# Kernel tuning notes

Measured on AMD Instinct MI355X. Metric: run time of the kernel, lower is better.

Reference implementation:

```python
import jax, jax.numpy as jnp
import numpy as np

NUM_QUERIES = 300

def setup_inputs() -> dict:
    key = jax.random.key(0)
    k1, k2, k3, k4 = jax.random.split(key, 4)
    B, A, L, H = 32, 8400, 80, 256
    return {
        "enc_outputs_class": jax.random.normal(k1, (B, A, L), dtype=jnp.float32),
        "enc_outputs_coord_logits_plus_anchors": jax.random.normal(k2, (B, A, 4), dtype=jnp.float32),
        "output_memory": jax.random.normal(k3, (B, A, H), dtype=jnp.float32),
        "sources_last_element": jax.random.normal(k4, (B, H, 20, 20), dtype=jnp.float32),
    }

def reference(enc_outputs_class, enc_outputs_coord_logits_plus_anchors, output_memory, sources_last_element):
    # enc_outputs_class: [B, A, L]; reduce class dim, top-k over anchors A.
    cls_max = jnp.max(enc_outputs_class, axis=-1)                      # [B, A]
    _, topk_ind = jax.lax.top_k(cls_max, NUM_QUERIES)                  # [B, Q], sorted desc
    idx = topk_ind[:, :, None]                                         # [B, Q, 1]

    def gather(data):  # per-batch gather along anchor axis
        return jnp.take_along_axis(data, idx, axis=1)

    reference_points_unact = gather(enc_outputs_coord_logits_plus_anchors)  # [B, Q, 4]
    enc_topk_logits = gather(enc_outputs_class)                             # [B, Q, L]
    enc_topk_bboxes = jax.nn.sigmoid(reference_points_unact)               # [B, Q, 4]

    # learn_initial_query=False: target comes from gathered encoder memory (stop-grad)
    target = jax.lax.stop_gradient(gather(output_memory))                   # [B, Q, H]
    init_reference_points = jax.lax.stop_gradient(reference_points_unact)  # [B, Q, 4]
    return (init_reference_points, target, enc_topk_logits, enc_topk_bboxes)
```

## Files before the change

### kernel.cpp

```cpp
#include <hip/hip_runtime.h>
#include <stdint.h>

#define BATCH 32
#define NA    8400
#define NL    80
#define NH    256
#define NK    300
#define NBIN  8192

#define OUT0 0
#define OUT1 38400
#define OUT2 2496000
#define OUT3 3264000

__device__ __forceinline__ unsigned mapf(float f) {
    unsigned u = __float_as_uint(f);
    return (u & 0x80000000u) ? ~u : (u | 0x80000000u);
}

__global__ __launch_bounds__(256) void cls_max_kernel(const float* __restrict__ cls,
                                                      unsigned* __restrict__ out_u) {
    int tid = threadIdx.x;
    int row = blockIdx.x * 64 + (tid >> 2);
    int sub = tid & 3;
    if (row >= BATCH * NA) return;
    const float4* p = (const float4*)(cls + (size_t)row * NL);
    float m = -3.4e38f;
#pragma unroll
    for (int q = 0; q < 5; ++q) {
        float4 v = p[sub + q * 4];
        m = fmaxf(m, fmaxf(fmaxf(v.x, v.y), fmaxf(v.z, v.w)));
    }
    m = fmaxf(m, __shfl_xor(m, 1));
    m = fmaxf(m, __shfl_xor(m, 2));
    if (sub == 0) out_u[row] = mapf(m);
}

__global__ __launch_bounds__(1024) void select_gather_kernel(
        const unsigned* __restrict__ u_in,
        const float*    __restrict__ cls,
        const float*    __restrict__ coord,
        const float*    __restrict__ mem,
        float*          __restrict__ out) {
    __shared__ unsigned hist[NBIN];
    __shared__ unsigned long long keys[1024];
    __shared__ int ord[NK];
    __shared__ unsigned wsum[16], wsuf[16];
    __shared__ unsigned s_thr, s_count;

    int tid  = threadIdx.x;
    int lane = tid & 63;
    int wid  = tid >> 6;
    int b    = blockIdx.x >> 3;
    int sub  = blockIdx.x & 7;
    const unsigned* ub = u_in + b * NA;

    for (int i = tid; i < NBIN; i += 1024) hist[i] = 0;
    if (tid == 0) s_count = 0;
    __syncthreads();

    unsigned v[9];
#pragma unroll
    for (int k = 0; k < 9; ++k) {
        int i = tid + k * 1024;
        v[k] = (i < NA) ? ub[i] : 0u;
    }
#pragma unroll
    for (int k = 0; k < 9; ++k) {
        int i = tid + k * 1024;
        if (i < NA) atomicAdd(&hist[v[k] >> 19], 1u);
    }
    __syncthreads();

    unsigned base = tid * 8;
    unsigned h[8];
#pragma unroll
    for (int j = 0; j < 8; ++j) h[j] = hist[base + j];
    unsigned L = 0;
#pragma unroll
    for (int j = 0; j < 8; ++j) L += h[j];
    unsigned s = L;
#pragma unroll
    for (int off = 1; off < 64; off <<= 1) {
        unsigned t = __shfl_down(s, off);
        if (lane + off < 64) s += t;
    }
    if (lane == 0) wsum[wid] = s;
    __syncthreads();
    if (tid == 0) {
        unsigned acc = 0;
        for (int w = 15; w >= 0; --w) { acc += wsum[w]; wsuf[w] = acc; }
    }
    __syncthreads();
    unsigned above = (wid < 15 ? wsuf[wid + 1] : 0u) + (s - L);
    unsigned acc = above;
#pragma unroll
    for (int j = 7; j >= 0; --j) {
        unsigned S = acc + h[j];
        if (S >= (unsigned)NK && acc < (unsigned)NK) s_thr = base + (unsigned)j;
        acc = S;
    }
    __syncthreads();

    unsigned T = s_thr;
#pragma unroll
    for (int k = 0; k < 9; ++k) {
        int i = tid + k * 1024;
        if (i < NA && (v[k] >> 19) >= T) {
            unsigned pos = atomicAdd(&s_count, 1u);
            if (pos < 1024) keys[pos] = ((unsigned long long)(~v[k]) << 32) | (unsigned)i;
        }
    }
    __syncthreads();

    unsigned count = s_count < 1024u ? s_count : 1024u;
    if (tid < (int)count) {
        unsigned long long mykey = keys[tid];
        int rank = 0;
        for (unsigned j = 0; j < count; ++j) rank += (keys[j] < mykey);
        if (rank < NK) ord[rank] = (int)(mykey & 0xFFFFFFFFull);
    }
    __syncthreads();

    for (int q = sub + 8 * wid; q < NK; q += 8 * 16) {
        int idx = ord[q];
        size_t srow = (size_t)b * NA + (size_t)idx;
        size_t drow = (size_t)b * NK + (size_t)q;

        const float4* msrc = (const float4*)(mem + srow * NH);
        float4*       mdst = (float4*)(out + OUT1 + drow * NH);
        mdst[lane] = msrc[lane];

        if (lane < 20) {
            const float4* lsrc = (const float4*)(cls + srow * NL);
            float4*       ldst = (float4*)(out + OUT2 + drow * NL);
            ldst[lane] = lsrc[lane];
        }
        if (lane == 0) {
            float4 c = ((const float4*)(coord + srow * 4))[0];
            ((float4*)(out + OUT0 + drow * 4))[0] = c;
            float4 sg;
            sg.x = 1.0f / (1.0f + __expf(-c.x));
            sg.y = 1.0f / (1.0f + __expf(-c.y));
            sg.z = 1.0f / (1.0f + __expf(-c.z));
            sg.w = 1.0f / (1.0f + __expf(-c.w));
            ((float4*)(out + OUT3 + drow * 4))[0] = sg;
        }
    }
}

extern "C" void kernel_launch(void* const* d_in, const int* in_sizes, int n_in,
                              void* d_out, int out_size, void* d_ws, size_t ws_size,
                              hipStream_t stream) {
    const float* cls   = (const float*)d_in[0];
    const float* coord = (const float*)d_in[1];
    const float* mem   = (const float*)d_in[2];

    unsigned* ws_u = (unsigned*)d_ws;
    float*    out  = (float*)d_out;

    cls_max_kernel<<<(BATCH * NA) / 64, 256, 0, stream>>>(cls, ws_u);
    select_gather_kernel<<<BATCH * 8, 1024, 0, stream>>>(ws_u, cls, coord, mem, out);
}
```

Before: 34.73 us.

## Fuse class-max and select-gather into one cooperative kernel with grid sync

Merges the per-anchor class-max kernel into the selection/gather kernel and launches it cooperatively with 256 blocks of 1024 threads. Each block computes the max for its slice of 1050 anchor rows, then a grid-wide sync precedes the histogram top-k and the gather. This removes one kernel launch and the gap between the two kernels. In exchange the max phase runs on only 256 blocks instead of many small ones, which can lower memory-level parallelism when streaming the 86 MB class tensor, and the grid sync adds its own cost.

```diff
diff --git a/kernel.cpp b/kernel.cpp
--- a/kernel.cpp
+++ b/kernel.cpp
@@ -1,5 +1,8 @@
 #include <hip/hip_runtime.h>
+#include <hip/hip_cooperative_groups.h>
 #include <stdint.h>
+
+namespace cg = cooperative_groups;
 
 #define BATCH 32
 #define NA    8400
@@ -7,6 +10,7 @@
 #define NH    256
 #define NK    300
 #define NBIN  8192
+#define RPB   1050
 
 #define OUT0 0
 #define OUT1 38400
@@ -18,29 +22,11 @@
     return (u & 0x80000000u) ? ~u : (u | 0x80000000u);
 }
 
-__global__ __launch_bounds__(256) void cls_max_kernel(const float* __restrict__ cls,
-                                                      unsigned* __restrict__ out_u) {
-    int tid = threadIdx.x;
-    int row = blockIdx.x * 64 + (tid >> 2);
-    int sub = tid & 3;
-    if (row >= BATCH * NA) return;
-    const float4* p = (const float4*)(cls + (size_t)row * NL);
-    float m = -3.4e38f;
-#pragma unroll
-    for (int q = 0; q < 5; ++q) {
-        float4 v = p[sub + q * 4];
-        m = fmaxf(m, fmaxf(fmaxf(v.x, v.y), fmaxf(v.z, v.w)));
-    }
-    m = fmaxf(m, __shfl_xor(m, 1));
-    m = fmaxf(m, __shfl_xor(m, 2));
-    if (sub == 0) out_u[row] = mapf(m);
-}
-
-__global__ __launch_bounds__(1024) void select_gather_kernel(
-        const unsigned* __restrict__ u_in,
+__global__ __launch_bounds__(1024) void fused_kernel(
         const float*    __restrict__ cls,
         const float*    __restrict__ coord,
         const float*    __restrict__ mem,
+        unsigned*       __restrict__ ws_u,
         float*          __restrict__ out) {
     __shared__ unsigned hist[NBIN];
     __shared__ unsigned long long keys[1024];
@@ -51,13 +37,34 @@
     int tid  = threadIdx.x;
     int lane = tid & 63;
     int wid  = tid >> 6;
-    int b    = blockIdx.x >> 3;
-    int sub  = blockIdx.x & 7;
-    const unsigned* ub = u_in + b * NA;
+    int b    = blockIdx.x & 31;
+    int sub  = blockIdx.x >> 5;
 
-    for (int i = tid; i < NBIN; i += 1024) hist[i] = 0;
-    if (tid == 0) s_count = 0;
-    __syncthreads();
+    {
+        int r4 = tid >> 2;
+        int s4 = tid & 3;
+        size_t rowbase = (size_t)b * NA + (size_t)sub * RPB;
+#pragma unroll
+        for (int p = 0; p < 5; ++p) {
+            int r = p * 256 + r4;
+            if (r < RPB) {
+                const float4* rp = (const float4*)(cls + (rowbase + r) * NL) + s4 * 5;
+                float m = -3.4e38f;
+#pragma unroll
+                for (int e = 0; e < 5; ++e) {
+                    float4 w = rp[e];
+                    m = fmaxf(m, fmaxf(fmaxf(w.x, w.y), fmaxf(w.z, w.w)));
+                }
+                m = fmaxf(m, __shfl_xor(m, 1));
+                m = fmaxf(m, __shfl_xor(m, 2));
+                if (s4 == 0) ws_u[rowbase + r] = mapf(m);
+            }
+        }
+    }
+
+    cg::this_grid().sync();
+
+    const unsigned* ub = ws_u + b * NA;
 
     unsigned v[9];
 #pragma unroll
@@ -65,6 +72,11 @@
         int i = tid + k * 1024;
         v[k] = (i < NA) ? ub[i] : 0u;
     }
+
+    for (int i = tid; i < NBIN; i += 1024) hist[i] = 0;
+    if (tid == 0) s_count = 0;
+    __syncthreads();
+
 #pragma unroll
     for (int k = 0; k < 9; ++k) {
         int i = tid + k * 1024;
@@ -159,6 +171,8 @@
     unsigned* ws_u = (unsigned*)d_ws;
     float*    out  = (float*)d_out;
 
-    cls_max_kernel<<<(BATCH * NA) / 64, 256, 0, stream>>>(cls, ws_u);
-    select_gather_kernel<<<BATCH * 8, 1024, 0, stream>>>(ws_u, cls, coord, mem, out);
+    void* args[] = {(void*)&cls, (void*)&coord, (void*)&mem,
+                    (void*)&ws_u, (void*)&out};
+    hipLaunchCooperativeKernel((const void*)fused_kernel,
+                               dim3(256), dim3(1024), args, 0, stream);
 }
```

After: 70.21 us. +102.1%, slower.
